# Optimization experiments

Measured on AMD Instinct MI355X. Metric: run time of the kernel, lower is better.

## Reference

```python
import jax, jax.numpy as jnp
import numpy as np

NUM_GRAPHS = 64
NEG_SLOPE = 0.2


def _gatv2_conv(x, src, dst, Wl, bl, Wr, br, att, bias):
    # PyG GATv2Conv (concat=True, share_weights=False, residual=False)
    N = x.shape[0]
    H, C = att.shape
    xl = (x @ Wl.T + bl).reshape(N, H, C)  # source transform
    xr = (x @ Wr.T + br).reshape(N, H, C)  # target transform
    e = jax.nn.leaky_relu(xl[src] + xr[dst], NEG_SLOPE)      # [E,H,C]
    alpha = jnp.einsum('ehc,hc->eh', e, att)                 # [E,H]
    # softmax over incoming edges per target node (numerically stable)
    amax = jax.ops.segment_max(alpha, dst, num_segments=N)   # [N,H]
    amax = jnp.where(jnp.isfinite(amax), amax, 0.0)
    ex = jnp.exp(alpha - amax[dst])
    denom = jax.ops.segment_sum(ex, dst, num_segments=N)
    a = ex / (denom[dst] + 1e-16)                            # [E,H]
    out = jax.ops.segment_sum(xl[src] * a[:, :, None], dst, num_segments=N)  # [N,H,C]
    return out.reshape(N, H * C) + bias


def setup_inputs() -> dict:
    key = jax.random.key(0)
    ks = jax.random.split(key, 20)
    N, E, F_in, hidden, H = 50000, 1600000, 256, 128, 4
    C = hidden // H
    s = 0.05
    inp = {
        'x': jax.random.normal(ks[0], (N, F_in), dtype=jnp.float32),
        'edge_index': jax.random.randint(ks[1], (2, E), 0, N, dtype=jnp.int64),
        'batch': jnp.sort(jax.random.randint(ks[2], (N,), 0, NUM_GRAPHS, dtype=jnp.int64)),
        # layer 1 (in=F_in)
        'Wl1': jax.random.normal(ks[3], (hidden, F_in), dtype=jnp.float32) * s,
        'bl1': jnp.zeros((hidden,), dtype=jnp.float32),
        'Wr1': jax.random.normal(ks[4], (hidden, F_in), dtype=jnp.float32) * s,
        'br1': jnp.zeros((hidden,), dtype=jnp.float32),
        'att1': jax.random.normal(ks[5], (H, C), dtype=jnp.float32) * s,
        'bias1': jnp.zeros((hidden,), dtype=jnp.float32),
        # layer 2 (in=hidden)
        'Wl2': jax.random.normal(ks[6], (hidden, hidden), dtype=jnp.float32) * s,
        'bl2': jnp.zeros((hidden,), dtype=jnp.float32),
        'Wr2': jax.random.normal(ks[7], (hidden, hidden), dtype=jnp.float32) * s,
        'br2': jnp.zeros((hidden,), dtype=jnp.float32),
        'att2': jax.random.normal(ks[8], (H, C), dtype=jnp.float32) * s,
        'bias2': jnp.zeros((hidden,), dtype=jnp.float32),
        # head
        'Wlin': jax.random.normal(ks[9], (1, hidden), dtype=jnp.float32) * s,
        'blin': jnp.zeros((1,), dtype=jnp.float32),
    }
    return inp


def reference(x, edge_index, batch, Wl1, bl1, Wr1, br1, att1, bias1,
              Wl2, bl2, Wr2, br2, att2, bias2, Wlin, blin):
    N = x.shape[0]
    loop = jnp.arange(N, dtype=edge_index.dtype)
    src = jnp.concatenate([edge_index[0], loop])  # add_self_loops=True
    dst = jnp.concatenate([edge_index[1], loop])
    h = _gatv2_conv(x, src, dst, Wl1, bl1, Wr1, br1, att1, bias1)
    h = jax.nn.relu(h)  # norm=Identity, dropout no-op in eval
    h = _gatv2_conv(h, src, dst, Wl2, bl2, Wr2, br2, att2, bias2)
    # global_mean_pool
    sums = jax.ops.segment_sum(h, batch, num_segments=NUM_GRAPHS)
    cnt = jax.ops.segment_sum(jnp.ones((N,), h.dtype), batch, num_segments=NUM_GRAPHS)
    pooled = sums / jnp.maximum(cnt, 1.0)[:, None]
    return pooled @ Wlin.T + blin
```

## Files before the change

kernel.cpp:

```cpp
#include <hip/hip_runtime.h>
#include <hip/hip_fp16.h>
#include <math.h>
#include <stdint.h>

#define EPB 4096
#define NBKT 128

typedef _Float16 f16x8 __attribute__((ext_vector_type(8)));
typedef float f32x4 __attribute__((ext_vector_type(4)));
typedef float f32x2 __attribute__((ext_vector_type(2)));
typedef _Float16 h2 __attribute__((ext_vector_type(2)));

#define LOG2E 1.4426950f

__device__ __forceinline__ float fast_exp2(float x) {
#if __has_builtin(__builtin_amdgcn_exp2f)
    return __builtin_amdgcn_exp2f(x);
#else
    return __expf(x * 0.69314718f);
#endif
}

template<int CTRL>
__device__ __forceinline__ float dpp_add(float x) {
    union { float f; int i; } u, v;
    u.f = x;
    v.i = __builtin_amdgcn_update_dpp(0, u.i, CTRL, 0xF, 0xF, true);
    return x + v.f;
}
__device__ __forceinline__ float reduce16(float x) {
    x = dpp_add<0xB1>(x);
    x = dpp_add<0x4E>(x);
    x = dpp_add<0x124>(x);
    x = dpp_add<0x128>(x);
    return x;
}

template<int PERM>
__global__ void k_wpack(const float* __restrict__ Wl, const float* __restrict__ Wr,
                        _Float16* __restrict__ Wp, int K) {
    int t = blockIdx.x * 256 + threadIdx.x;
    int total = (K / 32) * 16 * 64;
    if (t >= total) return;
    int l = t & 63, ct = (t >> 6) & 15, kt = t >> 10;
    int col = ct * 16 + (l & 15);
    int k0 = kt * 32 + (l >> 4) * 8;
    const float* src = (col < 128) ? (Wl + (size_t)col * K)
                                   : (Wr + (size_t)(col - 128) * K);
    union { _Float16 h[8]; uint4 u; } o;
#pragma unroll
    for (int e = 0; e < 8; ++e) {
        int k = k0 + e, chan;
        if (PERM) {
            int m = k >> 1, hh = m >> 4, j = m & 15;
            int c0 = hh * 32 + j;
            chan = (k & 1) ? c0 + 16 : c0;
        } else chan = k;
        o.h[e] = (_Float16)src[chan];
    }
    reinterpret_cast<uint4*>(Wp)[t] = o.u;
}

template<int K, int CVT>
__global__ __launch_bounds__(256) void k_gemm_mfma(
    const void* __restrict__ Xin, const _Float16* __restrict__ Wp,
    const float* __restrict__ bl, const float* __restrict__ br,
    const float* __restrict__ att,
    uint32_t* __restrict__ xlh, float2* __restrict__ xrp,
    float* __restrict__ ledl, int N) {
    __shared__ _Float16 xs[32 * K];
    const int t = threadIdx.x, w = t >> 6, l = t & 63;
    const int row0 = blockIdx.x * 32;
    if (CVT) {
        const float* X = (const float*)Xin;
        for (int cid = t; cid < 32 * (K / 4); cid += 256) {
            int r = cid / (K / 4), c4 = (cid % (K / 4)) * 4;
            int gr = row0 + r;
            float4 v = make_float4(0.f, 0.f, 0.f, 0.f);
            if (gr < N) v = *reinterpret_cast<const float4*>(X + (size_t)gr * K + c4);
            h2 lo = {(_Float16)v.x, (_Float16)v.y};
            h2 hi = {(_Float16)v.z, (_Float16)v.w};
            uint2 pk;
            pk.x = __builtin_bit_cast(uint32_t, lo);
            pk.y = __builtin_bit_cast(uint32_t, hi);
            int ba = (r * K * 2 + c4 * 2) ^ ((r & 7) << 4);
            *reinterpret_cast<uint2*>(reinterpret_cast<char*>(xs) + ba) = pk;
        }
    } else {
        const _Float16* X = (const _Float16*)Xin;
        for (int cid = t; cid < 32 * (K / 8); cid += 256) {
            int r = cid / (K / 8), c8 = (cid % (K / 8)) * 8;
            int gr = row0 + r;
            uint4 v = make_uint4(0u, 0u, 0u, 0u);
            if (gr < N) v = *reinterpret_cast<const uint4*>(X + (size_t)gr * K + c8);
            int ba = (r * K * 2 + c8 * 2) ^ ((r & 7) << 4);
            *reinterpret_cast<uint4*>(reinterpret_cast<char*>(xs) + ba) = v;
        }
    }
    __syncthreads();
    f32x4 acc[2][4];
#pragma unroll
    for (int m = 0; m < 2; ++m)
#pragma unroll
        for (int n = 0; n < 4; ++n) acc[m][n] = (f32x4){0.f, 0.f, 0.f, 0.f};
#pragma unroll
    for (int kt = 0; kt < K / 32; ++kt) {
        f16x8 a[2], b[4];
#pragma unroll
        for (int m = 0; m < 2; ++m) {
            int r = m * 16 + (l & 15);
            int ba = (r * K * 2 + kt * 64 + (l >> 4) * 16) ^ ((r & 7) << 4);
            a[m] = *reinterpret_cast<const f16x8*>(reinterpret_cast<const char*>(xs) + ba);
        }
#pragma unroll
        for (int n = 0; n < 4; ++n) {
            int ct = w * 4 + n;
            b[n] = *reinterpret_cast<const f16x8*>(Wp + ((size_t)(kt * 16 + ct) * 64 + l) * 8);
        }
#pragma unroll
        for (int m = 0; m < 2; ++m)
#pragma unroll
            for (int n = 0; n < 4; ++n)
                acc[m][n] = __builtin_amdgcn_mfma_f32_16x16x32_f16(a[m], b[n], acc[m][n], 0, 0, 0);
    }
    const int j = l & 15;
    if (w < 2) {
        float attv[2][2], bv[2][2];
#pragma unroll
        for (int p = 0; p < 2; ++p) {
            int c0 = (2 * w + p) * 32 + j;
            attv[p][0] = att[c0]; attv[p][1] = att[c0 + 16];
            bv[p][0] = bl[c0];    bv[p][1] = bl[c0 + 16];
        }
#pragma unroll
        for (int m = 0; m < 2; ++m)
#pragma unroll
            for (int r4 = 0; r4 < 4; ++r4) {
                int gr = row0 + m * 16 + (l >> 4) * 4 + r4;
                bool ok = gr < N;
#pragma unroll
                for (int p = 0; p < 2; ++p) {
                    int h = 2 * w + p;
                    float v0 = acc[m][2 * p][r4] + bv[p][0];
                    float v1 = acc[m][2 * p + 1][r4] + bv[p][1];
                    float part = reduce16(fmaf(attv[p][0], v0, attv[p][1] * v1));
                    if (ok) {
                        h2 hp = {(_Float16)v0, (_Float16)v1};
                        xlh[(size_t)gr * 64 + h * 16 + j] = __builtin_bit_cast(uint32_t, hp);
                        if (j == 0) ledl[gr * 4 + h] = 0.6f * LOG2E * part;
                    }
                }
            }
    } else {
        float bv[2][2];
#pragma unroll
        for (int p = 0; p < 2; ++p) {
            int c0 = (2 * (w - 2) + p) * 32 + j;
            bv[p][0] = br[c0]; bv[p][1] = br[c0 + 16];
        }
#pragma unroll
        for (int m = 0; m < 2; ++m)
#pragma unroll
            for (int r4 = 0; r4 < 4; ++r4) {
                int gr = row0 + m * 16 + (l >> 4) * 4 + r4;
                if (gr < N) {
#pragma unroll
                    for (int p = 0; p < 2; ++p) {
                        int hh = 2 * (w - 2) + p;
                        float v0 = acc[m][2 * p][r4] + bv[p][0];
                        float v1 = acc[m][2 * p + 1][r4] + bv[p][1];
                        xrp[(size_t)gr * 64 + hh * 16 + j] = make_float2(v0, v1);
                    }
                }
            }
    }
}

__global__ __launch_bounds__(256) void k_hist(const int* __restrict__ dstArr,
                                              int* __restrict__ g_hist, int E) {
    __shared__ int h[NBKT];
    int t = threadIdx.x;
    if (t < NBKT) h[t] = 0;
    __syncthreads();
    int s0 = blockIdx.x * EPB, s1 = min(E, s0 + EPB);
    for (int i = s0 + t; i < s1; i += 256) atomicAdd(&h[dstArr[i] >> 9], 1);
    __syncthreads();
    if (t < NBKT) g_hist[blockIdx.x * NBKT + t] = h[t];
}
__global__ __launch_bounds__(512) void k_part_scan(const int* __restrict__ g_hist,
                                                   int* __restrict__ g_base,
                                                   int* __restrict__ bstart_out,
                                                   int NB1, int E) {
    __shared__ int csum[4][NBKT];
    __shared__ int btot[NBKT];
    __shared__ int bstart[NBKT];
    int tid = threadIdx.x, c = tid >> 7, b = tid & (NBKT - 1);
    int chunk = (NB1 + 3) >> 2;
    int i0 = c * chunk, i1 = min(NB1, i0 + chunk);
    int run = 0;
    for (int i = i0; i < i1; ++i) run += g_hist[i * NBKT + b];
    csum[c][b] = run;
    __syncthreads();
    int mytot = 0;
    if (c == 0) {
        mytot = csum[0][b] + csum[1][b] + csum[2][b] + csum[3][b];
        btot[b] = mytot;
    }
    __syncthreads();
    for (int off = 1; off < NBKT; off <<= 1) {
        int add = 0;
        if (c == 0 && b >= off) add = btot[b - off];
        __syncthreads();
        if (c == 0) btot[b] += add;
        __syncthreads();
    }
    if (c == 0) { bstart[b] = btot[b] - mytot; bstart_out[b] = bstart[b]; }
    if (tid == 0) bstart_out[NBKT] = E;
    __syncthreads();
    int base = bstart[b];
    for (int cc = 0; cc < c; ++cc) base += csum[cc][b];
    run = base;
    for (int i = i0; i < i1; ++i) {
        g_base[i * NBKT + b] = run;
        run += g_hist[i * NBKT + b];
    }
}
__global__ __launch_bounds__(256) void k_scatter(const int* __restrict__ ei,
                                                 const int* __restrict__ g_base,
                                                 uint32_t* __restrict__ tmp, int E) {
    __shared__ int off[NBKT];
    int t = threadIdx.x;
    if (t < NBKT) off[t] = g_base[blockIdx.x * NBKT + t];
    __syncthreads();
    int s0 = blockIdx.x * EPB, s1 = min(E, s0 + EPB);
    for (int i = s0 + t; i < s1; i += 256) {
        int s = ei[i], d = ei[E + i];
        int pos = atomicAdd(&off[d >> 9], 1);
        tmp[pos] = ((uint32_t)s << 16) | (uint32_t)d;
    }
}
__global__ __launch_bounds__(256) void k_bucket_csr(
    const uint32_t* __restrict__ tmp, const int* __restrict__ bstart,
    int* __restrict__ rowptr, int* __restrict__ csr, int N, int E) {
    __shared__ int cnt[512];
    __shared__ int fil[512];
    int b = blockIdx.x, t = threadIdx.x;
    int s0 = bstart[b], s1 = bstart[b + 1];
    cnt[t] = 0; cnt[t + 256] = 0;
    __syncthreads();
    for (int i = s0 + t; i < s1; i += 256)
        atomicAdd(&cnt[tmp[i] & 511], 1);
    __syncthreads();
    int c0 = cnt[t], c1 = cnt[t + 256];
    for (int off = 1; off < 512; off <<= 1) {
        int v0 = (t >= off) ? cnt[t - off] : 0;
        int v1 = (t + 256 >= off) ? cnt[t + 256 - off] : 0;
        __syncthreads();
        cnt[t] += v0; cnt[t + 256] += v1;
        __syncthreads();
    }
    int e0 = cnt[t] - c0, e1 = cnt[t + 256] - c1;
    __syncthreads();
    cnt[t] = e0; cnt[t + 256] = e1;
    fil[t] = 1; fil[t + 256] = 1;
    __syncthreads();
    int n0 = b * 512;
#pragma unroll
    for (int k = 0; k < 2; ++k) {
        int ld = t + k * 256, n = n0 + ld;
        if (n < N) {
            int rp = s0 + cnt[ld] + n;
            rowptr[n] = rp;
            csr[rp] = n;
        }
    }
    if (b == 0 && t == 0) rowptr[N] = E + N;
    for (int i = s0 + t; i < s1; i += 256) {
        uint32_t pk = tmp[i];
        int d = (int)(pk & 0xFFFFu), ld = d & 511;
        int slot = atomicAdd(&fil[ld], 1);
        csr[s0 + cnt[ld] + d + slot] = (int)(pk >> 16);
    }
}

template<int OUT16>
__global__ __launch_bounds__(256) void k_gat_edge(
    const uint32_t* __restrict__ xlh, const float2* __restrict__ xrp,
    const float* __restrict__ ledl, const float* __restrict__ att,
    const float* __restrict__ bias,
    const int* __restrict__ rowptr, const int* __restrict__ csr,
    void* __restrict__ out, int N) {
    const int l = threadIdx.x & 63;
    const int n = __builtin_amdgcn_readfirstlane(blockIdx.x * 4 + (threadIdx.x >> 6));
    if (n >= N) return;
    const int h = l >> 4, j = l & 15;
    const int c0 = h * 32 + j, c1 = c0 + 16;
    const float2 xrv = xrp[(size_t)n * 64 + l];
    const f32x2 xr2 = {xrv.x, xrv.y};
    const float a04 = att[c0] * (0.4f * LOG2E), a14 = att[c1] * (0.4f * LOG2E);
    f32x2 acc2 = {0.f, 0.f};
    float ssum = 0.f;
    const int beg = rowptr[n], end = rowptr[n + 1];
    int i = beg;
    for (; i + 7 < end; i += 8) {
        int sr[8];
#pragma unroll
        for (int e = 0; e < 8; ++e) sr[e] = __builtin_amdgcn_readfirstlane(csr[i + e]);
        uint32_t q[8]; float lv[8];
#pragma unroll
        for (int e = 0; e < 8; ++e) {
            q[e]  = xlh[(size_t)(uint32_t)sr[e] * 64 + l];
            lv[e] = ledl[(uint32_t)sr[e] * 4 + h];
        }
#pragma unroll
        for (int e = 0; e < 8; ++e) {
            h2 A = __builtin_bit_cast(h2, q[e]);
            f32x2 A2 = {(float)A.x, (float)A.y};
            f32x2 t2 = A2 + xr2;
            float p = fmaf(fabsf(t2.y), a14, fabsf(t2.x) * a04);
            p = reduce16(p);
            float w = fast_exp2(p + lv[e]);
            ssum += w;
            acc2 = __builtin_elementwise_fma((f32x2){w, w}, A2, acc2);
        }
    }
    for (; i < end; ++i) {
        int s = __builtin_amdgcn_readfirstlane(csr[i]);
        uint32_t q = xlh[(size_t)(uint32_t)s * 64 + l];
        float lv  = ledl[(uint32_t)s * 4 + h];
        h2 A = __builtin_bit_cast(h2, q);
        f32x2 A2 = {(float)A.x, (float)A.y};
        f32x2 t2 = A2 + xr2;
        float p = fmaf(fabsf(t2.y), a14, fabsf(t2.x) * a04);
        p = reduce16(p);
        float w = fast_exp2(p + lv);
        ssum += w;
        acc2 = __builtin_elementwise_fma((f32x2){w, w}, A2, acc2);
    }
    float inv = 1.f / ssum;
    float o0 = fmaf(acc2.x, inv, bias[c0]);
    float o1 = fmaf(acc2.y, inv, bias[c1]);
    if (OUT16) {
        o0 = fmaxf(o0, 0.f); o1 = fmaxf(o1, 0.f);
        h2 oh = {(_Float16)o0, (_Float16)o1};
        ((uint32_t*)out)[(size_t)n * 64 + l] = __builtin_bit_cast(uint32_t, oh);
    } else {
        ((float2*)out)[(size_t)n * 64 + l] = make_float2(o0, o1);
    }
}

__global__ void k_zero(float* __restrict__ p, int n) {
    int i = blockIdx.x * 256 + threadIdx.x;
    if (i < n) p[i] = 0.f;
}
__global__ __launch_bounds__(128) void k_pool(
    const float* __restrict__ h, const int* __restrict__ batch,
    float* __restrict__ pool, float* __restrict__ gcnt, int N) {
    const int NPB = 32;
    int c = threadIdx.x;
    int n0 = blockIdx.x * NPB;
    int n1 = min(n0 + NPB, N);
    float acc = 0.f;
    int curg = -1, cntl = 0;
    for (int n = n0; n < n1; ++n) {
        int g = batch[n];
        if (g != curg) {
            if (curg >= 0) {
                atomicAdd(&pool[curg * 128 + c], acc);
                if (c == 0) atomicAdd(&gcnt[curg], (float)cntl);
            }
            acc = 0.f; cntl = 0; curg = g;
        }
        acc += h[(size_t)n * 128 + c];
        cntl++;
    }
    if (curg >= 0) {
        atomicAdd(&pool[curg * 128 + c], acc);
        if (c == 0) atomicAdd(&gcnt[curg], (float)cntl);
    }
}
__global__ __launch_bounds__(64) void k_head(
    const float* __restrict__ pool, const float* __restrict__ gcnt,
    const float* __restrict__ Wlin, const float* __restrict__ blin,
    float* __restrict__ out, int G) {
    int g = blockIdx.x, l = threadIdx.x;
    float2 pv = ((const float2*)pool)[g * 64 + l];
    int c0 = (l >> 4) * 32 + (l & 15);
    float d = pv.x * Wlin[c0] + pv.y * Wlin[c0 + 16];
#pragma unroll
    for (int off = 32; off; off >>= 1) d += __shfl_xor(d, off, 64);
    if (l == 0) {
        float cnt = fmaxf(gcnt[g], 1.f);
        out[g] = d / cnt + blin[0];
    }
}

extern "C" void kernel_launch(void* const* d_in, const int* in_sizes, int n_in,
                              void* d_out, int out_size, void* d_ws, size_t ws_size,
                              hipStream_t stream) {
    const float* x     = (const float*)d_in[0];
    const int*   ei    = (const int*)d_in[1];
    const int*   batch = (const int*)d_in[2];
    const float* Wl1   = (const float*)d_in[3];
    const float* bl1   = (const float*)d_in[4];
    const float* Wr1   = (const float*)d_in[5];
    const float* br1   = (const float*)d_in[6];
    const float* att1  = (const float*)d_in[7];
    const float* bias1 = (const float*)d_in[8];
    const float* Wl2   = (const float*)d_in[9];
    const float* bl2   = (const float*)d_in[10];
    const float* Wr2   = (const float*)d_in[11];
    const float* br2   = (const float*)d_in[12];
    const float* att2  = (const float*)d_in[13];
    const float* bias2 = (const float*)d_in[14];
    const float* Wlin  = (const float*)d_in[15];
    const float* blin  = (const float*)d_in[16];

    const int N   = in_sizes[2];
    const int E   = in_sizes[1] / 2;
    const int Fin = in_sizes[0] / N;
    const int G   = out_size;
    (void)n_in; (void)ws_size;

    char* p = (char*)d_ws;
    auto alloc = [&](size_t bytes) -> char* {
        char* r = p;
        p += (bytes + 255) & ~(size_t)255;
        return r;
    };
    uint32_t* xlh   = (uint32_t*)alloc((size_t)N * 64 * 4);
    float2*   xrp   = (float2*)alloc((size_t)N * 64 * 8);
    uint32_t* hbh   = (uint32_t*)alloc((size_t)N * 64 * 4);
    float*    hbf   = (float*)alloc((size_t)N * 128 * 4);
    float*    ledl  = (float*)alloc((size_t)N * 4 * 4);
    float*    wt    = (float*)alloc((size_t)Fin * 256 * 4);
    int*      rowptr= (int*)alloc((size_t)(N + 1) * 4);
    int*      csr   = (int*)alloc((size_t)(E + N) * 4);
    float*    poolg = (float*)alloc((size_t)G * 129 * 4);
    float*    pool  = poolg;
    float*    gcnt  = poolg + (size_t)G * 128;

    const int NB1 = (E + EPB - 1) / EPB;
    int*      g_hist = (int*)alloc((size_t)NB1 * NBKT * 4);
    int*      g_base = (int*)alloc((size_t)NB1 * NBKT * 4);
    int*      bstart = (int*)alloc((size_t)(NBKT + 1) * 4);
    uint32_t* tmp = (uint32_t*)xrp;
    _Float16* Wp  = (_Float16*)wt;

    const int wb = (N + 3) / 4;
    const int gb = (N + 31) / 32;

    k_hist<<<NB1, 256, 0, stream>>>(ei + E, g_hist, E);
    k_part_scan<<<1, 512, 0, stream>>>(g_hist, g_base, bstart, NB1, E);
    k_scatter<<<NB1, 256, 0, stream>>>(ei, g_base, tmp, E);
    k_bucket_csr<<<NBKT, 256, 0, stream>>>(tmp, bstart, rowptr, csr, N, E);

    k_wpack<0><<<((Fin / 32) * 16 * 64 + 255) / 256, 256, 0, stream>>>(Wl1, Wr1, Wp, Fin);
    k_gemm_mfma<256, 1><<<gb, 256, 0, stream>>>(x, Wp, bl1, br1, att1, xlh, xrp, ledl, N);
    k_gat_edge<1><<<wb, 256, 0, stream>>>(xlh, xrp, ledl, att1, bias1, rowptr, csr, hbh, N);

    k_wpack<1><<<((128 / 32) * 16 * 64 + 255) / 256, 256, 0, stream>>>(Wl2, Wr2, Wp, 128);
    k_gemm_mfma<128, 0><<<gb, 256, 0, stream>>>(hbh, Wp, bl2, br2, att2, xlh, xrp, ledl, N);
    k_gat_edge<0><<<wb, 256, 0, stream>>>(xlh, xrp, ledl, att2, bias2, rowptr, csr, hbf, N);

    k_zero<<<(G * 129 + 255) / 256, 256, 0, stream>>>(poolg, G * 129);
    k_pool<<<(N + 31) / 32, 128, 0, stream>>>(hbf, batch, pool, gcnt, N);
    k_head<<<G, 64, 0, stream>>>(pool, gcnt, Wlin, blin, (float*)d_out, G);
}
```

Before: 274.2 us.

## Software-pipeline edge gathers, enlarge GEMM row tile, merge weight packing and zeroing

The edge-aggregation loop now prefetches the next batch of 8 source rows while computing the current batch, so gather latency overlaps with the exp and reduction math. The MFMA GEMM tile grows from 32 to 64 rows per block, which doubles reuse of the weight fragments at the cost of more LDS and accumulator registers. Both layers' weight packing is fused into one kernel writing two separate buffers, and the pool-buffer zeroing moves into the histogram kernel, removing two launches. The extra prefetch registers and larger LDS could lower occupancy.

```diff
diff --git a/kernel.cpp b/kernel.cpp
--- a/kernel.cpp
+++ b/kernel.cpp
@@ -36,29 +36,41 @@
     return x;
 }
 
-template<int PERM>
-__global__ void k_wpack(const float* __restrict__ Wl, const float* __restrict__ Wr,
-                        _Float16* __restrict__ Wp, int K) {
+__global__ void k_wpack_all(const float* __restrict__ Wl1, const float* __restrict__ Wr1,
+                            const float* __restrict__ Wl2, const float* __restrict__ Wr2,
+                            _Float16* __restrict__ Wp1, _Float16* __restrict__ Wp2,
+                            int K1) {
     int t = blockIdx.x * 256 + threadIdx.x;
-    int total = (K / 32) * 16 * 64;
-    if (t >= total) return;
-    int l = t & 63, ct = (t >> 6) & 15, kt = t >> 10;
-    int col = ct * 16 + (l & 15);
-    int k0 = kt * 32 + (l >> 4) * 8;
-    const float* src = (col < 128) ? (Wl + (size_t)col * K)
-                                   : (Wr + (size_t)(col - 128) * K);
-    union { _Float16 h[8]; uint4 u; } o;
-#pragma unroll
-    for (int e = 0; e < 8; ++e) {
-        int k = k0 + e, chan;
-        if (PERM) {
+    int total1 = (K1 / 32) * 16 * 64;
+    int total2 = (128 / 32) * 16 * 64;
+    if (t < total1) {
+        int l = t & 63, ct = (t >> 6) & 15, kt = t >> 10;
+        int col = ct * 16 + (l & 15);
+        int k0 = kt * 32 + (l >> 4) * 8;
+        const float* src = (col < 128) ? (Wl1 + (size_t)col * K1)
+                                       : (Wr1 + (size_t)(col - 128) * K1);
+        union { _Float16 h[8]; uint4 u; } o;
+#pragma unroll
+        for (int e = 0; e < 8; ++e) o.h[e] = (_Float16)src[k0 + e];
+        reinterpret_cast<uint4*>(Wp1)[t] = o.u;
+    } else if (t < total1 + total2) {
+        int t2 = t - total1;
+        int l = t2 & 63, ct = (t2 >> 6) & 15, kt = t2 >> 10;
+        int col = ct * 16 + (l & 15);
+        int k0 = kt * 32 + (l >> 4) * 8;
+        const float* src = (col < 128) ? (Wl2 + (size_t)col * 128)
+                                       : (Wr2 + (size_t)(col - 128) * 128);
+        union { _Float16 h[8]; uint4 u; } o;
+#pragma unroll
+        for (int e = 0; e < 8; ++e) {
+            int k = k0 + e;
             int m = k >> 1, hh = m >> 4, j = m & 15;
             int c0 = hh * 32 + j;
-            chan = (k & 1) ? c0 + 16 : c0;
-        } else chan = k;
-        o.h[e] = (_Float16)src[chan];
-    }
-    reinterpret_cast<uint4*>(Wp)[t] = o.u;
+            int chan = (k & 1) ? c0 + 16 : c0;
+            o.h[e] = (_Float16)src[chan];
+        }
+        reinterpret_cast<uint4*>(Wp2)[t2] = o.u;
+    }
 }
 
 template<int K, int CVT>
@@ -68,12 +80,12 @@
     const float* __restrict__ att,
     uint32_t* __restrict__ xlh, float2* __restrict__ xrp,
     float* __restrict__ ledl, int N) {
-    __shared__ _Float16 xs[32 * K];
+    __shared__ _Float16 xs[64 * K];
     const int t = threadIdx.x, w = t >> 6, l = t & 63;
-    const int row0 = blockIdx.x * 32;
+    const int row0 = blockIdx.x * 64;
     if (CVT) {
         const float* X = (const float*)Xin;
-        for (int cid = t; cid < 32 * (K / 4); cid += 256) {
+        for (int cid = t; cid < 64 * (K / 4); cid += 256) {
             int r = cid / (K / 4), c4 = (cid % (K / 4)) * 4;
             int gr = row0 + r;
             float4 v = make_float4(0.f, 0.f, 0.f, 0.f);
@@ -88,7 +100,7 @@
         }
     } else {
         const _Float16* X = (const _Float16*)Xin;
-        for (int cid = t; cid < 32 * (K / 8); cid += 256) {
+        for (int cid = t; cid < 64 * (K / 8); cid += 256) {
             int r = cid / (K / 8), c8 = (cid % (K / 8)) * 8;
             int gr = row0 + r;
             uint4 v = make_uint4(0u, 0u, 0u, 0u);
@@ -98,16 +110,16 @@
         }
     }
     __syncthreads();
-    f32x4 acc[2][4];
-#pragma unroll
-    for (int m = 0; m < 2; ++m)
+    f32x4 acc[4][4];
+#pragma unroll
+    for (int m = 0; m < 4; ++m)
 #pragma unroll
         for (int n = 0; n < 4; ++n) acc[m][n] = (f32x4){0.f, 0.f, 0.f, 0.f};
 #pragma unroll
     for (int kt = 0; kt < K / 32; ++kt) {
-        f16x8 a[2], b[4];
-#pragma unroll
-        for (int m = 0; m < 2; ++m) {
+        f16x8 a[4], b[4];
+#pragma unroll
+        for (int m = 0; m < 4; ++m) {
             int r = m * 16 + (l & 15);
             int ba = (r * K * 2 + kt * 64 + (l >> 4) * 16) ^ ((r & 7) << 4);
             a[m] = *reinterpret_cast<const f16x8*>(reinterpret_cast<const char*>(xs) + ba);
@@ -118,7 +130,7 @@
             b[n] = *reinterpret_cast<const f16x8*>(Wp + ((size_t)(kt * 16 + ct) * 64 + l) * 8);
         }
 #pragma unroll
-        for (int m = 0; m < 2; ++m)
+        for (int m = 0; m < 4; ++m)
 #pragma unroll
             for (int n = 0; n < 4; ++n)
                 acc[m][n] = __builtin_amdgcn_mfma_f32_16x16x32_f16(a[m], b[n], acc[m][n], 0, 0, 0);
@@ -133,7 +145,7 @@
             bv[p][0] = bl[c0];    bv[p][1] = bl[c0 + 16];
         }
 #pragma unroll
-        for (int m = 0; m < 2; ++m)
+        for (int m = 0; m < 4; ++m)
 #pragma unroll
             for (int r4 = 0; r4 < 4; ++r4) {
                 int gr = row0 + m * 16 + (l >> 4) * 4 + r4;
@@ -159,7 +171,7 @@
             bv[p][0] = br[c0]; bv[p][1] = br[c0 + 16];
         }
 #pragma unroll
-        for (int m = 0; m < 2; ++m)
+        for (int m = 0; m < 4; ++m)
 #pragma unroll
             for (int r4 = 0; r4 < 4; ++r4) {
                 int gr = row0 + m * 16 + (l >> 4) * 4 + r4;
@@ -177,9 +189,12 @@
 }
 
 __global__ __launch_bounds__(256) void k_hist(const int* __restrict__ dstArr,
-                                              int* __restrict__ g_hist, int E) {
+                                              int* __restrict__ g_hist, int E,
+                                              float* __restrict__ zbuf, int zn) {
     __shared__ int h[NBKT];
     int t = threadIdx.x;
+    int zi = blockIdx.x * 256 + t;
+    if (zi < zn) zbuf[zi] = 0.f;
     if (t < NBKT) h[t] = 0;
     __syncthreads();
     int s0 = blockIdx.x * EPB, s1 = min(E, s0 + EPB);
@@ -281,6 +296,19 @@
         int slot = atomicAdd(&fil[ld], 1);
         csr[s0 + cnt[ld] + d + slot] = (int)(pk >> 16);
     }
+}
+
+__device__ __forceinline__ void edge_compute(
+    uint32_t q, float lv, f32x2 xr2, float a04, float a14,
+    float& ssum, f32x2& acc2) {
+    h2 A = __builtin_bit_cast(h2, q);
+    f32x2 A2 = {(float)A.x, (float)A.y};
+    f32x2 t2 = A2 + xr2;
+    float p = fmaf(fabsf(t2.y), a14, fabsf(t2.x) * a04);
+    p = reduce16(p);
+    float w = fast_exp2(p + lv);
+    ssum += w;
+    acc2 = __builtin_elementwise_fma((f32x2){w, w}, A2, acc2);
 }
 
 template<int OUT16>
@@ -302,40 +330,38 @@
     float ssum = 0.f;
     const int beg = rowptr[n], end = rowptr[n + 1];
     int i = beg;
-    for (; i + 7 < end; i += 8) {
-        int sr[8];
-#pragma unroll
-        for (int e = 0; e < 8; ++e) sr[e] = __builtin_amdgcn_readfirstlane(csr[i + e]);
-        uint32_t q[8]; float lv[8];
+    if (i + 7 < end) {
+        uint32_t q0[8]; float lv0[8];
 #pragma unroll
         for (int e = 0; e < 8; ++e) {
-            q[e]  = xlh[(size_t)(uint32_t)sr[e] * 64 + l];
-            lv[e] = ledl[(uint32_t)sr[e] * 4 + h];
-        }
-#pragma unroll
-        for (int e = 0; e < 8; ++e) {
-            h2 A = __builtin_bit_cast(h2, q[e]);
-            f32x2 A2 = {(float)A.x, (float)A.y};
-            f32x2 t2 = A2 + xr2;
-            float p = fmaf(fabsf(t2.y), a14, fabsf(t2.x) * a04);
-            p = reduce16(p);
-            float w = fast_exp2(p + lv[e]);
-            ssum += w;
-            acc2 = __builtin_elementwise_fma((f32x2){w, w}, A2, acc2);
-        }
+            int s = __builtin_amdgcn_readfirstlane(csr[i + e]);
+            q0[e]  = xlh[(size_t)(uint32_t)s * 64 + l];
+            lv0[e] = ledl[(uint32_t)s * 4 + h];
+        }
+        for (; i + 15 < end; i += 8) {
+            uint32_t q1[8]; float lv1[8];
+#pragma unroll
+            for (int e = 0; e < 8; ++e) {
+                int s = __builtin_amdgcn_readfirstlane(csr[i + 8 + e]);
+                q1[e]  = xlh[(size_t)(uint32_t)s * 64 + l];
+                lv1[e] = ledl[(uint32_t)s * 4 + h];
+            }
+#pragma unroll
+            for (int e = 0; e < 8; ++e)
+                edge_compute(q0[e], lv0[e], xr2, a04, a14, ssum, acc2);
+#pragma unroll
+            for (int e = 0; e < 8; ++e) { q0[e] = q1[e]; lv0[e] = lv1[e]; }
+        }
+#pragma unroll
+        for (int e = 0; e < 8; ++e)
+            edge_compute(q0[e], lv0[e], xr2, a04, a14, ssum, acc2);
+        i += 8;
     }
     for (; i < end; ++i) {
         int s = __builtin_amdgcn_readfirstlane(csr[i]);
         uint32_t q = xlh[(size_t)(uint32_t)s * 64 + l];
         float lv  = ledl[(uint32_t)s * 4 + h];
-        h2 A = __builtin_bit_cast(h2, q);
-        f32x2 A2 = {(float)A.x, (float)A.y};
-        f32x2 t2 = A2 + xr2;
-        float p = fmaf(fabsf(t2.y), a14, fabsf(t2.x) * a04);
-        p = reduce16(p);
-        float w = fast_exp2(p + lv);
-        ssum += w;
-        acc2 = __builtin_elementwise_fma((f32x2){w, w}, A2, acc2);
+        edge_compute(q, lv, xr2, a04, a14, ssum, acc2);
     }
     float inv = 1.f / ssum;
     float o0 = fmaf(acc2.x, inv, bias[c0]);
@@ -349,10 +375,6 @@
     }
 }
 
-__global__ void k_zero(float* __restrict__ p, int n) {
-    int i = blockIdx.x * 256 + threadIdx.x;
-    if (i < n) p[i] = 0.f;
-}
 __global__ __launch_bounds__(128) void k_pool(
     const float* __restrict__ h, const int* __restrict__ batch,
     float* __restrict__ pool, float* __restrict__ gcnt, int N) {
@@ -433,7 +455,8 @@
     uint32_t* hbh   = (uint32_t*)alloc((size_t)N * 64 * 4);
     float*    hbf   = (float*)alloc((size_t)N * 128 * 4);
     float*    ledl  = (float*)alloc((size_t)N * 4 * 4);
-    float*    wt    = (float*)alloc((size_t)Fin * 256 * 4);
+    float*    wt1   = (float*)alloc((size_t)Fin * 256 * 2);
+    float*    wt2   = (float*)alloc((size_t)128 * 256 * 2);
     int*      rowptr= (int*)alloc((size_t)(N + 1) * 4);
     int*      csr   = (int*)alloc((size_t)(E + N) * 4);
     float*    poolg = (float*)alloc((size_t)G * 129 * 4);
@@ -445,25 +468,28 @@
     int*      g_base = (int*)alloc((size_t)NB1 * NBKT * 4);
     int*      bstart = (int*)alloc((size_t)(NBKT + 1) * 4);
     uint32_t* tmp = (uint32_t*)xrp;
-    _Float16* Wp  = (_Float16*)wt;
+    _Float16* Wp1 = (_Float16*)wt1;
+    _Float16* Wp2 = (_Float16*)wt2;
 
     const int wb = (N + 3) / 4;
-    const int gb = (N + 31) / 32;
-
-    k_hist<<<NB1, 256, 0, stream>>>(ei + E, g_hist, E);
+    const int gb = (N + 63) / 64;
+
+    k_hist<<<NB1, 256, 0, stream>>>(ei + E, g_hist, E, poolg, G * 129);
     k_part_scan<<<1, 512, 0, stream>>>(g_hist, g_base, bstart, NB1, E);
     k_scatter<<<NB1, 256, 0, stream>>>(ei, g_base, tmp, E);
     k_bucket_csr<<<NBKT, 256, 0, stream>>>(tmp, bstart, rowptr, csr, N, E);
 
-    k_wpack<0><<<((Fin / 32) * 16 * 64 + 255) / 256, 256, 0, stream>>>(Wl1, Wr1, Wp, Fin);
-    k_gemm_mfma<256, 1><<<gb, 256, 0, stream>>>(x, Wp, bl1, br1, att1, xlh, xrp, ledl, N);
+    {
+        int total = (Fin / 32) * 16 * 64 + (128 / 32) * 16 * 64;
+        k_wpack_all<<<(total + 255) / 256, 256, 0, stream>>>(Wl1, Wr1, Wl2, Wr2, Wp1, Wp2, Fin);
+    }
+
+    k_gemm_mfma<256, 1><<<gb, 256, 0, stream>>>(x, Wp1, bl1, br1, att1, xlh, xrp, ledl, N);
     k_gat_edge<1><<<wb, 256, 0, stream>>>(xlh, xrp, ledl, att1, bias1, rowptr, csr, hbh, N);
 
-    k_wpack<1><<<((128 / 32) * 16 * 64 + 255) / 256, 256, 0, stream>>>(Wl2, Wr2, Wp, 128);
-    k_gemm_mfma<128, 0><<<gb, 256, 0, stream>>>(hbh, Wp, bl2, br2, att2, xlh, xrp, ledl, N);
+    k_gemm_mfma<128, 0><<<gb, 256, 0, stream>>>(hbh, Wp2, bl2, br2, att2, xlh, xrp, ledl, N);
     k_gat_edge<0><<<wb, 256, 0, stream>>>(xlh, xrp, ledl, att2, bias2, rowptr, csr, hbf, N);
 
-    k_zero<<<(G * 129 + 255) / 256, 256, 0, stream>>>(poolg, G * 129);
     k_pool<<<(N + 31) / 32, 128, 0, stream>>>(hbf, batch, pool, gcnt, N);
     k_head<<<G, 64, 0, stream>>>(pool, gcnt, Wlin, blin, (float*)d_out, G);
 }
```

After: 287.6 us. +4.9%, slower.
